# Kernel tuning notes

Hardware: AMD Instinct MI355X
Metric: run time of the kernel (lower is better)

Reference implementation:

```python
import jax, jax.numpy as jnp
import numpy as np

BS, NINP, NHID, K, T = 2048, 512, 512, 16, 8
M = NHID // K  # per-block hidden = 32
ATT_D = 16     # read/write key dim
TAU = 0.5


def setup_inputs() -> dict:
    key = jax.random.key(0)
    ks = jax.random.split(key, 10)
    s = 0.1
    return {
        "x": jax.random.normal(ks[0], (BS, NINP), jnp.float32),
        "h": jax.random.normal(ks[1], (BS, NHID), jnp.float32),
        # stacked GRUCell params across templates (torch gate order: r, z, n)
        "W_ih": jax.random.normal(ks[2], (T, 3 * M, NINP), jnp.float32) * s,
        "W_hh": jax.random.normal(ks[3], (T, 3 * M, M), jnp.float32) * s,
        "b_ih": jax.random.normal(ks[4], (T, 3 * M), jnp.float32) * s,
        "b_hh": jax.random.normal(ks[5], (T, 3 * M), jnp.float32) * s,
        # GroupLinearLayer weights (no bias): read has 1 group, write has T groups
        "w_read": jax.random.normal(ks[6], (1, M, ATT_D), jnp.float32) * s,
        "w_write": jax.random.normal(ks[7], (T, M, ATT_D), jnp.float32) * s,
        # pre-sampled Gumbel noise for gumbel_softmax, shape [bs*k, T]
        "gumbel_noise": jax.random.gumbel(ks[8], (BS * K, T), jnp.float32),
    }


def reference(x, h, W_ih, W_hh, b_ih, b_hh, w_read, w_write, gumbel_noise):
    bs = h.shape[0]
    N = bs * K
    # blockify hidden: [bs, nhid] -> [N, m]
    h2 = h.reshape(N, M)
    # tile input across blocks: [bs, ninp] -> [N, ninp]
    xin = jnp.broadcast_to(x[:, None, :], (bs, K, NINP)).reshape(N, NINP)
    # read key: GroupLinearLayer with 1 group -> [N, ATT_D]
    h_read = h2 @ w_read[0]
    # all-template GRUCell as two grouped GEMMs: [T, N, 3m]
    gi = jnp.einsum('ni,tgi->tng', xin, W_ih) + b_ih[:, None, :]
    gh = jnp.einsum('nm,tgm->tng', h2, W_hh) + b_hh[:, None, :]
    r = jax.nn.sigmoid(gi[..., :M] + gh[..., :M])
    z = jax.nn.sigmoid(gi[..., M:2 * M] + gh[..., M:2 * M])
    n = jnp.tanh(gi[..., 2 * M:] + r * gh[..., 2 * M:])
    hnext = (1.0 - z) * n + z * h2[None]            # [T, N, m]
    hnext = hnext.transpose(1, 0, 2)                # [N, T, m]
    # write keys: grouped linear per template -> [N, T, ATT_D]
    write_key = jnp.einsum('ntm,tmf->ntf', hnext, w_write)
    # attention logits: bmm(h_read[N,1,f], write_key^T) -> [N, T]
    logits = jnp.einsum('nf,ntf->nt', h_read, write_key)
    # hard gumbel-softmax (tau=0.5) with straight-through estimator
    y_soft = jax.nn.softmax((logits + gumbel_noise) / TAU, axis=-1)
    y_hard = jax.nn.one_hot(jnp.argmax(y_soft, axis=-1), T, dtype=y_soft.dtype)
    att = y_hard + y_soft - jax.lax.stop_gradient(y_soft)  # [N, T]
    # combine templates (bmm with [N,1,T] then mean over singleton dim)
    h_out = jnp.einsum('nt,ntm->nm', att, hnext)    # [N, m]
    h_out = h_out.reshape(bs, K * M)
    att_out = jax.lax.stop_gradient(att).reshape(bs, K, T)
    return h_out, att_out
```

## Files before the change

kernel.cpp:

```cpp
#include <hip/hip_runtime.h>

#define NB_BS   2048
#define NB_NINP 512
#define NB_NHID 512
#define NB_K    16
#define NB_T    8
#define NB_M    32
#define NB_C    768
#define H_OUT_ELEMS (NB_BS * NB_NHID)

__global__ __launch_bounds__(1024)
void k1_gemm_gi(const float* __restrict__ x, const float* __restrict__ Wih,
                const float* __restrict__ bih, const float* __restrict__ bhh,
                float* __restrict__ gi)
{
    __shared__ __align__(16) float As[4][16][68];
    __shared__ __align__(16) float Bs[4][16][100];
    __shared__ float ACCX[256][25];

    const int tid  = threadIdx.x;
    const int kg   = tid >> 8;
    const int ttid = tid & 255;
    const int row0 = blockIdx.x * 64;
    const int col0 = blockIdx.y * 96;
    const int rg   = ttid >> 4;
    const int cg   = ttid & 15;
    const int kb0  = kg * 128;

    const int ar = ttid >> 2, akq = (ttid & 3) * 4;
    const int bc0 = ttid >> 2,              bk0 = (ttid & 3) * 4;
    const int bc1 = (256 + ttid) >> 2,      bk1 = (ttid & 3) * 4;

    float4 a0 = *(const float4*)&x[(size_t)(row0 + ar) * NB_NINP + kb0 + akq];
    float4 b0 = *(const float4*)&Wih[(size_t)(col0 + bc0) * NB_NINP + kb0 + bk0];
    float4 b1;
    if (ttid < 128)
        b1 = *(const float4*)&Wih[(size_t)(col0 + bc1) * NB_NINP + kb0 + bk1];

    float acc[4][6];
    #pragma unroll
    for (int i = 0; i < 4; ++i)
        #pragma unroll
        for (int e = 0; e < 6; ++e) acc[i][e] = 0.f;

    for (int slab = 0; slab < 8; ++slab) {
        __syncthreads();
        As[kg][akq+0][ar]=a0.x; As[kg][akq+1][ar]=a0.y;
        As[kg][akq+2][ar]=a0.z; As[kg][akq+3][ar]=a0.w;
        Bs[kg][bk0+0][bc0]=b0.x; Bs[kg][bk0+1][bc0]=b0.y;
        Bs[kg][bk0+2][bc0]=b0.z; Bs[kg][bk0+3][bc0]=b0.w;
        if (ttid < 128) {
            Bs[kg][bk1+0][bc1]=b1.x; Bs[kg][bk1+1][bc1]=b1.y;
            Bs[kg][bk1+2][bc1]=b1.z; Bs[kg][bk1+3][bc1]=b1.w;
        }
        __syncthreads();
        if (slab < 7) {
            const int kb = kb0 + (slab + 1) * 16;
            a0 = *(const float4*)&x[(size_t)(row0 + ar) * NB_NINP + kb + akq];
            b0 = *(const float4*)&Wih[(size_t)(col0 + bc0) * NB_NINP + kb + bk0];
            if (ttid < 128)
                b1 = *(const float4*)&Wih[(size_t)(col0 + bc1) * NB_NINP + kb + bk1];
        }
        #pragma unroll
        for (int kk = 0; kk < 16; ++kk) {
            const float4 av = *(const float4*)&As[kg][kk][rg * 4];
            const float2 w0 = *(const float2*)&Bs[kg][kk][cg * 6];
            const float2 w1 = *(const float2*)&Bs[kg][kk][cg * 6 + 2];
            const float2 w2 = *(const float2*)&Bs[kg][kk][cg * 6 + 4];
            const float avv[4] = {av.x, av.y, av.z, av.w};
            const float wvv[6] = {w0.x, w0.y, w1.x, w1.y, w2.x, w2.y};
            #pragma unroll
            for (int i = 0; i < 4; ++i)
                #pragma unroll
                for (int e = 0; e < 6; ++e)
                    acc[i][e] = fmaf(avv[i], wvv[e], acc[i][e]);
        }
    }

    #pragma unroll 1
    for (int src = 1; src < 4; ++src) {
        __syncthreads();
        if (kg == src) {
            #pragma unroll
            for (int i = 0; i < 4; ++i)
                #pragma unroll
                for (int e = 0; e < 6; ++e) ACCX[ttid][i * 6 + e] = acc[i][e];
        }
        __syncthreads();
        if (kg == 0) {
            #pragma unroll
            for (int i = 0; i < 4; ++i)
                #pragma unroll
                for (int e = 0; e < 6; ++e) acc[i][e] += ACCX[ttid][i * 6 + e];
        }
    }
    if (kg == 0) {
        float bias[6];
        #pragma unroll
        for (int e = 0; e < 6; ++e) {
            const int cl = cg * 6 + e;
            const int c  = col0 + cl;
            bias[e] = bih[c] + (cl < 64 ? bhh[c] : 0.f);
        }
        #pragma unroll
        for (int i = 0; i < 4; ++i) {
            const size_t base = (size_t)(row0 + rg * 4 + i) * NB_C + col0 + cg * 6;
            #pragma unroll
            for (int e = 0; e < 6; e += 2) {
                float2 o;
                o.x = acc[i][e]   + bias[e];
                o.y = acc[i][e+1] + bias[e+1];
                *(float2*)&gi[base + e] = o;
            }
        }
    }
}

__global__ __launch_bounds__(1024)
__attribute__((amdgpu_waves_per_eu(4, 4)))
void k2_fused(const float* __restrict__ h,      const float* __restrict__ Whh,
              const float* __restrict__ bhh,    const float* __restrict__ wread,
              const float* __restrict__ wwrite, const float* __restrict__ gumb,
              const float* __restrict__ gi,     float* __restrict__ out)
{
    __shared__ __align__(16) float4 P[3][32][64];
    __shared__ __align__(16) float4 WWT4[16][64];
    __shared__ __align__(16) float WR[512];
    __shared__ __align__(16) float HT[8][32][20];
    __shared__ __align__(16) float HR2T[8][16][20];
    __shared__ __align__(16) float LG[8][16][8];

    const int tid  = threadIdx.x;
    const int wave = tid >> 6, lane = tid & 63;
    const int bl   = wave >> 1, kh = wave & 1;
    const int b    = blockIdx.x * 8 + bl;
    const int m_   = lane & 31, half = lane >> 5;

    float* PF = (float*)P;
    for (int i = tid; i < 24576; i += 1024) {
        const int c = i >> 5, mm = i & 31;
        const int t = c / 96, rem = c - t * 96;
        const int gc = rem >> 5, mout = rem & 31;
        const int j  = (t >> 1) * 3 + gc;
        const int sl = ((t & 1) * 32 + mout) ^ (mm & 7);
        PF[(((j >> 2) * 32 + mm) * 64 + sl) * 4 + (j & 3)] = Whh[i];
    }
    for (int i = tid; i < 4096; i += 1024) {
        const int t = i >> 9, mo = (i >> 4) & 31, f = i & 15;
        ((float*)WWT4)[(f * 64 + (t & 1) * 32 + mo) * 4 + (t >> 1)] = wwrite[i];
    }
    if (tid < 512) WR[tid] = wread[tid];
    #pragma unroll
    for (int e = 0; e < 4; ++e) {
        const int idx = kh * 256 + e * 64 + lane;
        HT[bl][idx & 31][idx >> 5] = h[(size_t)b * NB_NHID + idx];
    }
    __syncthreads();

    {
        const int kq = kh * 8 + (lane >> 3);
        const int f0 = (lane & 7) * 2;
        float s0 = 0.f, s1 = 0.f;
        #pragma unroll 8
        for (int mm = 0; mm < 32; ++mm) {
            const float hv = HT[bl][mm][kq];
            s0 = fmaf(hv, WR[mm * 16 + f0], s0);
            s1 = fmaf(hv, WR[mm * 16 + f0 + 1], s1);
        }
        HR2T[bl][f0    ][kq] = s0;
        HR2T[bl][f0 + 1][kq] = s1;
    }

    float gi_r[4][3], bhn[4];
    #pragma unroll
    for (int p = 0; p < 4; ++p) {
        const int t = 2 * p + half;
        #pragma unroll
        for (int gc = 0; gc < 3; ++gc)
            gi_r[p][gc] = gi[(size_t)b * NB_C + t * 96 + gc * 32 + m_];
        bhn[p] = bhh[t * 96 + 64 + m_];
    }

    #pragma unroll 1
    for (int pass = 0; pass < 2; ++pass) {
        const int k0 = kh * 8 + pass * 4;

        float acc[4][12];
        #pragma unroll
        for (int r = 0; r < 4; ++r)
            #pragma unroll
            for (int j = 0; j < 12; ++j) acc[r][j] = 0.f;

        __builtin_amdgcn_s_setprio(1);
        #pragma unroll 4
        for (int mm = 0; mm < 32; ++mm) {
            const int sw = lane ^ (mm & 7);
            const float4 w0 = P[0][mm][sw];
            const float4 w1 = P[1][mm][sw];
            const float4 w2 = P[2][mm][sw];
            const float4 hv = *(const float4*)&HT[bl][mm][k0];
            const float wj[12] = {w0.x,w0.y,w0.z,w0.w, w1.x,w1.y,w1.z,w1.w,
                                  w2.x,w2.y,w2.z,w2.w};
            const float hr4[4] = {hv.x, hv.y, hv.z, hv.w};
            #pragma unroll
            for (int r = 0; r < 4; ++r)
                #pragma unroll
                for (int j = 0; j < 12; ++j)
                    acc[r][j] = fmaf(hr4[r], wj[j], acc[r][j]);
        }
        __builtin_amdgcn_s_setprio(0);

        float ww[4][4];
        #pragma unroll
        for (int r = 0; r < 4; ++r)
            #pragma unroll
            for (int p = 0; p < 4; ++p) ww[r][p] = 0.f;
        #pragma unroll 4
        for (int f = 0; f < 16; ++f) {
            const float4 wt4 = WWT4[f][half * 32 + m_];
            const float4 hka = *(const float4*)&HR2T[bl][f][k0];
            const float wt[4] = {wt4.x, wt4.y, wt4.z, wt4.w};
            const float hk[4] = {hka.x, hka.y, hka.z, hka.w};
            #pragma unroll
            for (int r = 0; r < 4; ++r)
                #pragma unroll
                for (int p = 0; p < 4; ++p)
                    ww[r][p] = fmaf(hk[r], wt[p], ww[r][p]);
        }

        #pragma unroll
        for (int r = 0; r < 4; ++r) {
            const int k = k0 + r;
            const float h2v = HT[bl][m_][k];
            float hn[4], part[4];
            #pragma unroll
            for (int p = 0; p < 4; ++p) {
                const float xr = gi_r[p][0] + acc[r][p*3+0];
                const float xz = gi_r[p][1] + acc[r][p*3+1];
                const float gn = bhn[p]     + acc[r][p*3+2];
                const float rg = 1.f / (1.f + __expf(-xr));
                const float zg = 1.f / (1.f + __expf(-xz));
                const float xn = gi_r[p][2] + rg * gn;
                const float e2 = __expf(2.f * xn);
                const float tn = 1.f - 2.f / (e2 + 1.f);
                const float hv2 = (1.f - zg) * tn + zg * h2v;
                hn[p] = hv2;
                part[p] = hv2 * ww[r][p];
            }
            #pragma unroll
            for (int p = 0; p < 4; ++p)
                part[p] += __shfl_xor(part[p], 16, 64);
            const bool b4 = (lane & 16) != 0, b3 = (lane & 8) != 0;
            float v01 = b4 ? part[1] : part[0];
            float v23 = b4 ? part[3] : part[2];
            v01 += __shfl_xor(v01, 8, 64);
            v23 += __shfl_xor(v23, 8, 64);
            float v = b3 ? v23 : v01;
            v += __shfl_xor(v, 4, 64);
            v += __shfl_xor(v, 2, 64);
            v += __shfl_xor(v, 1, 64);
            if ((lane & 7) == 0) {
                const int p_ = ((lane >> 4) & 1) | (((lane >> 3) & 1) << 1);
                LG[bl][k][2 * p_ + half] = v;
            }
            const float4 l0 = *(const float4*)&LG[bl][k][0];
            const float4 l1 = *(const float4*)&LG[bl][k][4];
            const float* gp = gumb + ((size_t)b * NB_K + k) * NB_T;
            const float4 ga = *(const float4*)gp;
            const float4 gb = *(const float4*)(gp + 4);
            const float s[8] = {l0.x+ga.x, l0.y+ga.y, l0.z+ga.z, l0.w+ga.w,
                                l1.x+gb.x, l1.y+gb.y, l1.z+gb.z, l1.w+gb.w};
            float best = s[0]; int bt = 0;
            #pragma unroll
            for (int t2 = 1; t2 < 8; ++t2)
                if (s[t2] > best) { best = s[t2]; bt = t2; }
            const int pstar = bt >> 1, hstar = bt & 1;
            float hsel = hn[0];
            hsel = (pstar == 1) ? hn[1] : hsel;
            hsel = (pstar == 2) ? hn[2] : hsel;
            hsel = (pstar == 3) ? hn[3] : hsel;
            if (half == hstar)
                out[(size_t)b * NB_NHID + k * 32 + m_] = hsel;
            if (lane < 8)
                out[H_OUT_ELEMS + ((size_t)b * NB_K + k) * NB_T + lane] =
                    (lane == bt) ? 1.f : 0.f;
        }
    }
}

extern "C" void kernel_launch(void* const* d_in, const int* in_sizes, int n_in,
                              void* d_out, int out_size, void* d_ws, size_t ws_size,
                              hipStream_t stream) {
    const float* x      = (const float*)d_in[0];
    const float* h      = (const float*)d_in[1];
    const float* Wih    = (const float*)d_in[2];
    const float* Whh    = (const float*)d_in[3];
    const float* bih    = (const float*)d_in[4];
    const float* bhh    = (const float*)d_in[5];
    const float* wread  = (const float*)d_in[6];
    const float* wwrite = (const float*)d_in[7];
    const float* gumb   = (const float*)d_in[8];
    float* out = (float*)d_out;
    float* gi  = (float*)d_ws;

    k1_gemm_gi<<<dim3(32, 8), 1024, 0, stream>>>(x, Wih, bih, bhh, gi);
    k2_fused<<<dim3(256), 1024, 0, stream>>>(h, Whh, bhh, wread, wwrite,
                                             gumb, gi, out);
}
```

Before: 79.00 us.

## Split-K the input GEMM across blocks and reduce partials in fused kernel

Replaces the single 1024-thread in-block split-K GEMM with a 3D grid of 256-thread blocks, each computing one K-quarter and writing its partial sum to a separate workspace slice. The second kernel sums the four partials when it loads gi. This raises the block count for more CU occupancy and removes the in-block shared-memory reduction. In exchange it writes and reads four times as much gi data through global memory and needs a larger workspace; the old path remains as a fallback when the workspace is too small.

```diff
diff --git a/kernel.cpp b/kernel.cpp
--- a/kernel.cpp
+++ b/kernel.cpp
@@ -8,6 +8,96 @@
 #define NB_M    32
 #define NB_C    768
 #define H_OUT_ELEMS (NB_BS * NB_NHID)
+#define GI_ELEMS (NB_BS * NB_C)
+
+__global__ __launch_bounds__(256, 4)
+void k1_part(const float* __restrict__ x, const float* __restrict__ Wih,
+             const float* __restrict__ bih, const float* __restrict__ bhh,
+             float* __restrict__ gp)
+{
+    __shared__ __align__(16) float As[32][68];
+    __shared__ __align__(16) float Bs[32][100];
+
+    const int tid  = threadIdx.x;
+    const int row0 = blockIdx.x * 64;
+    const int col0 = blockIdx.y * 96;
+    const int kz   = blockIdx.z;
+    const int kb0  = kz * 128;
+    const int rg   = tid >> 4;
+    const int cg   = tid & 15;
+
+    const int ar0 = tid >> 3, akq = (tid & 7) * 4, ar1 = ar0 + 32;
+    const int c0 = tid >> 3, c1 = c0 + 32, c2 = c0 + 64;
+
+    float4 a0 = *(const float4*)&x[(size_t)(row0 + ar0) * NB_NINP + kb0 + akq];
+    float4 a1 = *(const float4*)&x[(size_t)(row0 + ar1) * NB_NINP + kb0 + akq];
+    float4 b0 = *(const float4*)&Wih[(size_t)(col0 + c0) * NB_NINP + kb0 + akq];
+    float4 b1 = *(const float4*)&Wih[(size_t)(col0 + c1) * NB_NINP + kb0 + akq];
+    float4 b2 = *(const float4*)&Wih[(size_t)(col0 + c2) * NB_NINP + kb0 + akq];
+
+    float acc[4][6];
+    #pragma unroll
+    for (int i = 0; i < 4; ++i)
+        #pragma unroll
+        for (int e = 0; e < 6; ++e) acc[i][e] = 0.f;
+
+    for (int slab = 0; slab < 4; ++slab) {
+        __syncthreads();
+        As[akq+0][ar0]=a0.x; As[akq+1][ar0]=a0.y;
+        As[akq+2][ar0]=a0.z; As[akq+3][ar0]=a0.w;
+        As[akq+0][ar1]=a1.x; As[akq+1][ar1]=a1.y;
+        As[akq+2][ar1]=a1.z; As[akq+3][ar1]=a1.w;
+        Bs[akq+0][c0]=b0.x; Bs[akq+1][c0]=b0.y;
+        Bs[akq+2][c0]=b0.z; Bs[akq+3][c0]=b0.w;
+        Bs[akq+0][c1]=b1.x; Bs[akq+1][c1]=b1.y;
+        Bs[akq+2][c1]=b1.z; Bs[akq+3][c1]=b1.w;
+        Bs[akq+0][c2]=b2.x; Bs[akq+1][c2]=b2.y;
+        Bs[akq+2][c2]=b2.z; Bs[akq+3][c2]=b2.w;
+        __syncthreads();
+        if (slab < 3) {
+            const int kb = kb0 + (slab + 1) * 32;
+            a0 = *(const float4*)&x[(size_t)(row0 + ar0) * NB_NINP + kb + akq];
+            a1 = *(const float4*)&x[(size_t)(row0 + ar1) * NB_NINP + kb + akq];
+            b0 = *(const float4*)&Wih[(size_t)(col0 + c0) * NB_NINP + kb + akq];
+            b1 = *(const float4*)&Wih[(size_t)(col0 + c1) * NB_NINP + kb + akq];
+            b2 = *(const float4*)&Wih[(size_t)(col0 + c2) * NB_NINP + kb + akq];
+        }
+        #pragma unroll
+        for (int kk = 0; kk < 32; ++kk) {
+            const float4 av = *(const float4*)&As[kk][rg * 4];
+            const float2 w0 = *(const float2*)&Bs[kk][cg * 6];
+            const float2 w1 = *(const float2*)&Bs[kk][cg * 6 + 2];
+            const float2 w2 = *(const float2*)&Bs[kk][cg * 6 + 4];
+            const float avv[4] = {av.x, av.y, av.z, av.w};
+            const float wvv[6] = {w0.x, w0.y, w1.x, w1.y, w2.x, w2.y};
+            #pragma unroll
+            for (int i = 0; i < 4; ++i)
+                #pragma unroll
+                for (int e = 0; e < 6; ++e)
+                    acc[i][e] = fmaf(avv[i], wvv[e], acc[i][e]);
+        }
+    }
+
+    float bias[6];
+    #pragma unroll
+    for (int e = 0; e < 6; ++e) {
+        const int cl = cg * 6 + e;
+        const int c  = col0 + cl;
+        bias[e] = (kz == 0) ? (bih[c] + (cl < 64 ? bhh[c] : 0.f)) : 0.f;
+    }
+    float* go = gp + (size_t)kz * GI_ELEMS;
+    #pragma unroll
+    for (int i = 0; i < 4; ++i) {
+        const size_t base = (size_t)(row0 + rg * 4 + i) * NB_C + col0 + cg * 6;
+        #pragma unroll
+        for (int e = 0; e < 6; e += 2) {
+            float2 o;
+            o.x = acc[i][e]   + bias[e];
+            o.y = acc[i][e+1] + bias[e+1];
+            *(float2*)&go[base + e] = o;
+        }
+    }
+}
 
 __global__ __launch_bounds__(1024)
 void k1_gemm_gi(const float* __restrict__ x, const float* __restrict__ Wih,
@@ -28,8 +118,8 @@
     const int kb0  = kg * 128;
 
     const int ar = ttid >> 2, akq = (ttid & 3) * 4;
-    const int bc0 = ttid >> 2,              bk0 = (ttid & 3) * 4;
-    const int bc1 = (256 + ttid) >> 2,      bk1 = (ttid & 3) * 4;
+    const int bc0 = ttid >> 2,         bk0 = (ttid & 3) * 4;
+    const int bc1 = (256 + ttid) >> 2, bk1 = (ttid & 3) * 4;
 
     float4 a0 = *(const float4*)&x[(size_t)(row0 + ar) * NB_NINP + kb0 + akq];
     float4 b0 = *(const float4*)&Wih[(size_t)(col0 + bc0) * NB_NINP + kb0 + bk0];
@@ -121,7 +211,8 @@
 void k2_fused(const float* __restrict__ h,      const float* __restrict__ Whh,
               const float* __restrict__ bhh,    const float* __restrict__ wread,
               const float* __restrict__ wwrite, const float* __restrict__ gumb,
-              const float* __restrict__ gi,     float* __restrict__ out)
+              const float* __restrict__ gi,     const int nz,
+              float* __restrict__ out)
 {
     __shared__ __align__(16) float4 P[3][32][64];
     __shared__ __align__(16) float4 WWT4[16][64];
@@ -174,11 +265,17 @@
     float gi_r[4][3], bhn[4];
     #pragma unroll
     for (int p = 0; p < 4; ++p) {
-        const int t = 2 * p + half;
-        #pragma unroll
-        for (int gc = 0; gc < 3; ++gc)
-            gi_r[p][gc] = gi[(size_t)b * NB_C + t * 96 + gc * 32 + m_];
-        bhn[p] = bhh[t * 96 + 64 + m_];
+        #pragma unroll
+        for (int gc = 0; gc < 3; ++gc) gi_r[p][gc] = 0.f;
+        bhn[p] = bhh[(2 * p + half) * 96 + 64 + m_];
+    }
+    for (int z = 0; z < nz; ++z) {
+        const float* g = gi + (size_t)z * GI_ELEMS + (size_t)b * NB_C;
+        #pragma unroll
+        for (int p = 0; p < 4; ++p)
+            #pragma unroll
+            for (int gc = 0; gc < 3; ++gc)
+                gi_r[p][gc] += g[(2 * p + half) * 96 + gc * 32 + m_];
     }
 
     #pragma unroll 1
@@ -303,7 +400,14 @@
     float* out = (float*)d_out;
     float* gi  = (float*)d_ws;
 
-    k1_gemm_gi<<<dim3(32, 8), 1024, 0, stream>>>(x, Wih, bih, bhh, gi);
-    k2_fused<<<dim3(256), 1024, 0, stream>>>(h, Whh, bhh, wread, wwrite,
-                                             gumb, gi, out);
+    const bool split = (ws_size >= (size_t)4 * GI_ELEMS * sizeof(float));
+    if (split) {
+        k1_part<<<dim3(32, 8, 4), 256, 0, stream>>>(x, Wih, bih, bhh, gi);
+        k2_fused<<<dim3(256), 1024, 0, stream>>>(h, Whh, bhh, wread, wwrite,
+                                                 gumb, gi, 4, out);
+    } else {
+        k1_gemm_gi<<<dim3(32, 8), 1024, 0, stream>>>(x, Wih, bih, bhh, gi);
+        k2_fused<<<dim3(256), 1024, 0, stream>>>(h, Whh, bhh, wread, wwrite,
+                                                 gumb, gi, 1, out);
+    }
 }
```

Result: slower. 83.82 us (+6.1%).
